# Optimization experiments

Hardware: AMD Instinct MI355X
Metric: run time of the kernel (lower is better)

Reference implementation:

```python
import jax, jax.numpy as jnp
import numpy as np

K = 3
STRIDE = 1
PAD = 1
DIL = 1


def _conv(x, w, b):
    # x: [B,C,H,W], w: [O,C,K,K] (OIHW)
    y = jax.lax.conv_general_dilated(
        x, w, window_strides=(STRIDE, STRIDE),
        padding=[(PAD, PAD), (PAD, PAD)],
        dimension_numbers=("NCHW", "OIHW", "NCHW"))
    return y + b[None, :, None, None]


def _bilinear(img, py, px):
    # img: [B,C,H,W]; py,px: [B,Ho,Wo] float sample coords; zero outside.
    B, C, H, W = img.shape
    y0 = jnp.floor(py)
    x0 = jnp.floor(px)
    wy = py - y0
    wx = px - x0

    def gather(yi, xi):
        valid = (yi >= 0) & (yi < H) & (xi >= 0) & (xi < W)
        yc = jnp.clip(yi, 0, H - 1).astype(jnp.int32)
        xc = jnp.clip(xi, 0, W - 1).astype(jnp.int32)
        v = jax.vmap(lambda im, yy, xx: im[:, yy, xx])(img, yc, xc)  # [B,C,Ho,Wo]
        return v * valid[:, None, :, :].astype(img.dtype)

    v00 = gather(y0, x0)
    v01 = gather(y0, x0 + 1)
    v10 = gather(y0 + 1, x0)
    v11 = gather(y0 + 1, x0 + 1)
    wy_ = wy[:, None]
    wx_ = wx[:, None]
    return ((1 - wy_) * (1 - wx_) * v00 + (1 - wy_) * wx_ * v01
            + wy_ * (1 - wx_) * v10 + wy_ * wx_ * v11)


def setup_inputs() -> dict:
    key = jax.random.key(0)
    ks = jax.random.split(key, 7)
    B, Cin, Cout, H, W = 16, 96, 96, 128, 128
    n = Cin * K * K
    stdv = 1.0 / np.sqrt(n)
    x = jax.random.normal(ks[0], (B, Cin, H, W), jnp.float32)
    weight = jax.random.uniform(ks[1], (Cout, Cin, K, K), jnp.float32, -stdv, stdv)
    bias = jnp.zeros((Cout,), jnp.float32)
    # offset/mask convs: small random weights so sampling offsets are nontrivial
    offset_w = jax.random.normal(ks[2], (2 * K * K, Cin, K, K), jnp.float32) * 0.01
    offset_b = jax.random.normal(ks[3], (2 * K * K,), jnp.float32) * 0.1
    mask_w = jax.random.normal(ks[4], (K * K, Cin, K, K), jnp.float32) * 0.01
    mask_b = jnp.zeros((K * K,), jnp.float32)
    return {"x": x, "weight": weight, "bias": bias,
            "offset_w": offset_w, "offset_b": offset_b,
            "mask_w": mask_w, "mask_b": mask_b}


def reference(x, weight, bias, offset_w, offset_b, mask_w, mask_b):
    offset = _conv(x, offset_w, offset_b)              # [B, 2*K*K, Ho, Wo]
    mask = jax.nn.sigmoid(_conv(x, mask_w, mask_b))    # [B, K*K, Ho, Wo]
    B, C, H, W = x.shape
    Ho, Wo = offset.shape[2], offset.shape[3]
    base_y = (jnp.arange(Ho) * STRIDE - PAD).astype(x.dtype)  # output-row base coord
    base_x = (jnp.arange(Wo) * STRIDE - PAD).astype(x.dtype)
    out = jnp.zeros((B, weight.shape[0], Ho, Wo), x.dtype)
    for k in range(K * K):  # fixed small loop over kernel taps
        i, j = k // K, k % K
        dy = offset[:, 2 * k]      # torchvision ordering: (dy, dx) per tap
        dx = offset[:, 2 * k + 1]
        py = base_y[None, :, None] + i * DIL + dy   # [B,Ho,Wo]
        px = base_x[None, None, :] + j * DIL + dx
        samp = _bilinear(x, py, px) * mask[:, k][:, None]  # [B,C,Ho,Wo]
        out = out + jnp.einsum("bchw,oc->bohw", samp, weight[:, :, i, j])
    return out + bias[None, :, None, None]
```

## Files before the change

### kernel.cpp

```cpp
#include <hip/hip_runtime.h>
#include <math.h>

#define W 128
#define H 128
#define HW 16384
#define CIN 96
#define COUT 96
#define BATCH 16
#define NPIX (BATCH * HW)
#define BPITCH 104
#define BTAP (COUT * BPITCH)
#define BSTG 10240
#define NOT (27 * 32 * 32)

typedef __bf16 bf16x8 __attribute__((ext_vector_type(8)));
typedef float f32x4 __attribute__((ext_vector_type(4)));
typedef unsigned int u32x4 __attribute__((ext_vector_type(4)));

typedef const unsigned int __attribute__((address_space(1))) gu32;
typedef unsigned int __attribute__((address_space(3))) lu32;
#define GLDS16(g, l) __builtin_amdgcn_global_load_lds((gu32*)(g), (lu32*)(l), 16, 0, 0)

__device__ inline float bflo(unsigned d) { union { unsigned u; float f; } t; t.u = d << 16; return t.f; }
__device__ inline float bfhi(unsigned d) { union { unsigned u; float f; } t; t.u = d & 0xffff0000u; return t.f; }

__global__ void prep_weights(const float* __restrict__ weight,
                             const float* __restrict__ offset_w,
                             const float* __restrict__ mask_w,
                             __bf16* __restrict__ wOT,
                             __bf16* __restrict__ wBTp) {
  int idx = blockIdx.x * blockDim.x + threadIdx.x;
  if (idx < NOT) {
    int c = idx & 31;
    int o = (idx >> 5) & 31;
    int ks = idx >> 10;
    int tap = ks / 3;
    int cg = (ks % 3) * 32 + c;
    float v = 0.f;
    if (o < 18)      v = offset_w[(o * CIN + cg) * 9 + tap];
    else if (o < 27) v = mask_w[((o - 18) * CIN + cg) * 9 + tap];
    wOT[idx] = (__bf16)v;
  } else {
    int j = idx - NOT;
    if (j < 9 * BTAP + 256) {
      int c = j % BPITCH;
      int o = (j / BPITCH) % COUT;
      int tap = j / BTAP;
      float v = 0.f;
      if (tap < 9 && c < CIN) v = weight[(o * CIN + c) * 9 + tap];
      wBTp[j] = (__bf16)v;
    }
  }
}

__global__ __launch_bounds__(256) void nhwc_kernel(const float* __restrict__ x,
                                                   __bf16* __restrict__ xT) {
  int tid = blockIdx.x * 256 + threadIdx.x;
  int b = tid >> 14, pix = tid & (HW - 1);
  const float* xp = x + (size_t)b * CIN * HW + pix;
  __bf16* op = xT + (size_t)tid * CIN;
#pragma unroll
  for (int c0 = 0; c0 < CIN; c0 += 8) {
    bf16x8 v;
#pragma unroll
    for (int j = 0; j < 8; ++j) v[j] = (__bf16)xp[(size_t)(c0 + j) * HW];
    *(bf16x8*)(op + c0) = v;
  }
}

#define OISS_TAP(TAP, G) {                                                    \
    int ki = (TAP) / 3, kj = (TAP) % 3;                                       \
    int yy = h + ki - 1, xx = wg + kj - 1;                                    \
    bool ok = ((unsigned)yy < (unsigned)H) && ((unsigned)xx < (unsigned)W);   \
    unsigned vo = ok ? (unsigned)((yy * W + xx) * 192) + choff : 0x7f000000u; \
    asm volatile("buffer_load_dwordx4 %0, %1, %2, %3 offen"                   \
                 : "=v"(G[0]) : "v"(vo), "s"(rsrcX), "s"(0));                 \
    asm volatile("buffer_load_dwordx4 %0, %1, %2, %3 offen"                   \
                 : "=v"(G[1]) : "v"(vo), "s"(rsrcX), "s"(64));                \
    asm volatile("buffer_load_dwordx4 %0, %1, %2, %3 offen"                   \
                 : "=v"(G[2]) : "v"(vo), "s"(rsrcX), "s"(128));               \
  }

#define OISS_B(TAP)                                                           \
  _Pragma("unroll") for (int s = 0; s < 3; ++s)                               \
  _Pragma("unroll") for (int nt = 0; nt < 2; ++nt)                            \
    asm volatile("buffer_load_dwordx4 %0, %1, %2, %3 offen"                   \
                 : "=v"(bb[s * 2 + nt])                                       \
                 : "v"(voffB), "s"(rsrcW),                                    \
                   "s"((TAP) * 6144 + s * 2048 + nt * 1024));

#define OCOMP(GC)                                                             \
  _Pragma("unroll") for (int s = 0; s < 3; ++s) {                             \
    bf16x8 a = __builtin_bit_cast(bf16x8, GC[s]);                             \
    acc[0] = __builtin_amdgcn_mfma_f32_16x16x32_bf16(                         \
        a, __builtin_bit_cast(bf16x8, bb[s * 2 + 0]), acc[0], 0, 0, 0);       \
    acc[1] = __builtin_amdgcn_mfma_f32_16x16x32_bf16(                         \
        a, __builtin_bit_cast(bf16x8, bb[s * 2 + 1]), acc[1], 0, 0, 0);       \
  }

__global__ __launch_bounds__(256) void offmask_mfma(
    const __bf16* __restrict__ xT, const __bf16* __restrict__ wOT,
    const float* __restrict__ offset_b, const float* __restrict__ mask_b,
    float* __restrict__ offm) {
  int t = threadIdx.x;
  int lane = t & 63;
  int wv = __builtin_amdgcn_readfirstlane(t >> 6);
  int ln15 = lane & 15;

  int bid = (int)blockIdx.x;
  int nb = (bid & 7) * 512 + (bid >> 3);
  int b = nb >> 8;
  int rem = nb & 255;
  int h = rem >> 1;
  int w0 = (rem & 1) << 6;

  int pl = (wv << 4) + ln15;
  int wg = w0 + pl;
  unsigned choff = (unsigned)((lane >> 4) << 4);

  const __bf16* xb = xT + (size_t)b * HW * CIN;

  unsigned long long ba = (unsigned long long)(const void*)xb;
  u32x4 rsrcX;
  rsrcX.x = (unsigned)ba; rsrcX.y = (unsigned)(ba >> 32);
  rsrcX.z = (unsigned)(HW * 192);
  rsrcX.w = 0x00020000u;
  unsigned long long bwo = (unsigned long long)(const void*)wOT;
  u32x4 rsrcW;
  rsrcW.x = (unsigned)bwo; rsrcW.y = (unsigned)(bwo >> 32);
  rsrcW.z = (unsigned)(NOT * 2);
  rsrcW.w = 0x00020000u;
  unsigned voffB = (unsigned)(ln15 * 64 + ((lane >> 4) << 4));

  f32x4 acc[2];
  acc[0] = (f32x4){0.f, 0.f, 0.f, 0.f};
  acc[1] = (f32x4){0.f, 0.f, 0.f, 0.f};

  u32x4 gA[3], gB[3], bb[6];

  OISS_TAP(0, gA);
#pragma unroll
  for (int tap = 0; tap < 9; ++tap) {
    OISS_B(tap);
    if (tap < 8) {
      if (tap & 1) { OISS_TAP(tap + 1, gA); } else { OISS_TAP(tap + 1, gB); }
      asm volatile("s_waitcnt vmcnt(3)" ::: "memory");
    } else {
      asm volatile("s_waitcnt vmcnt(0)" ::: "memory");
    }
    __builtin_amdgcn_sched_barrier(0);
    if (tap & 1) { OCOMP(gB); } else { OCOMP(gA); }
  }

  float* ob = offm + (size_t)b * 27 * HW + (size_t)h * W;
  int prow = w0 + (wv << 4) + ((lane >> 4) << 2);
  {
    float bv = offset_b[ln15];
    float4 o4;
    o4.x = acc[0][0] + bv; o4.y = acc[0][1] + bv;
    o4.z = acc[0][2] + bv; o4.w = acc[0][3] + bv;
    *(float4*)(ob + (size_t)ln15 * HW + prow) = o4;
  }
  if (ln15 < 11) {
    int o = 16 + ln15;
    bool sig = (o >= 18);
    float bv = sig ? mask_b[o - 18] : offset_b[o];
    float4 o4;
    float v0 = acc[1][0] + bv, v1 = acc[1][1] + bv;
    float v2 = acc[1][2] + bv, v3 = acc[1][3] + bv;
    if (sig) {
      v0 = 1.f / (1.f + expf(-v0)); v1 = 1.f / (1.f + expf(-v1));
      v2 = 1.f / (1.f + expf(-v2)); v3 = 1.f / (1.f + expf(-v3));
    }
    o4.x = v0; o4.y = v1; o4.z = v2; o4.w = v3;
    *(float4*)(ob + (size_t)o * HW + prow) = o4;
  }
}

#define GISS(K, G, WD) {                                                      \
    float dyv = offt[2 * (K)][pl];                                            \
    float dxv = offt[2 * (K) + 1][pl];                                        \
    float mv  = offt[18 + (K)][pl];                                           \
    int ki = (K) / 3, kj = (K) % 3;                                           \
    float py = (float)(h - 1 + ki) + dyv;                                     \
    float px = (float)(wg - 1 + kj) + dxv;                                    \
    float fy = floorf(py), fx = floorf(px);                                   \
    float wyf = py - fy, wxf = px - fx;                                       \
    int iy0 = (int)fy, ix0 = (int)fx;                                         \
    int iy1 = iy0 + 1, ix1 = ix0 + 1;                                         \
    bool y0ok = (unsigned)iy0 < (unsigned)H;                                  \
    bool y1ok = (unsigned)iy1 < (unsigned)H;                                  \
    bool x0ok = (unsigned)ix0 < (unsigned)W;                                  \
    bool x1ok = (unsigned)ix1 < (unsigned)W;                                  \
    WD[0] = (y0ok && x0ok) ? (1.f - wyf) * (1.f - wxf) * mv : 0.f;            \
    WD[1] = (y0ok && x1ok) ? (1.f - wyf) * wxf * mv : 0.f;                    \
    WD[2] = (y1ok && x0ok) ? wyf * (1.f - wxf) * mv : 0.f;                    \
    WD[3] = (y1ok && x1ok) ? wyf * wxf * mv : 0.f;                            \
    int cy0 = min(max(iy0, 0), H - 1), cy1 = min(max(iy1, 0), H - 1);         \
    int cx0 = min(max(ix0, 0), W - 1), cx1 = min(max(ix1, 0), W - 1);         \
    unsigned v00 = (unsigned)((cy0 * W + cx0) * 192) + choff;                 \
    unsigned v01 = (unsigned)((cy0 * W + cx1) * 192) + choff;                 \
    unsigned v10 = (unsigned)((cy1 * W + cx0) * 192) + choff;                 \
    unsigned v11 = (unsigned)((cy1 * W + cx1) * 192) + choff;                 \
    _Pragma("unroll") for (int ks = 0; ks < 3; ++ks) {                        \
      asm volatile("buffer_load_dwordx4 %0, %1, %2, %3 offen"                 \
                   : "=v"(G[ks * 4 + 0]) : "v"(v00), "s"(rsrcX), "s"(ks * 64)); \
      asm volatile("buffer_load_dwordx4 %0, %1, %2, %3 offen"                 \
                   : "=v"(G[ks * 4 + 1]) : "v"(v01), "s"(rsrcX), "s"(ks * 64)); \
      asm volatile("buffer_load_dwordx4 %0, %1, %2, %3 offen"                 \
                   : "=v"(G[ks * 4 + 2]) : "v"(v10), "s"(rsrcX), "s"(ks * 64)); \
      asm volatile("buffer_load_dwordx4 %0, %1, %2, %3 offen"                 \
                   : "=v"(G[ks * 4 + 3]) : "v"(v11), "s"(rsrcX), "s"(ks * 64)); \
    } }

#define COMBINE_KS(G, KS, WV, AF)                                             \
  _Pragma("unroll") for (int j = 0; j < 8; ++j) {                             \
    unsigned d00 = G[(KS) * 4 + 0][j >> 1], d01 = G[(KS) * 4 + 1][j >> 1];    \
    unsigned d10 = G[(KS) * 4 + 2][j >> 1], d11 = G[(KS) * 4 + 3][j >> 1];    \
    float v00 = (j & 1) ? bfhi(d00) : bflo(d00);                              \
    float v01 = (j & 1) ? bfhi(d01) : bflo(d01);                              \
    float v10 = (j & 1) ? bfhi(d10) : bflo(d10);                              \
    float v11 = (j & 1) ? bfhi(d11) : bflo(d11);                              \
    AF[j] = (__bf16)(WV[0] * v00 + WV[1] * v01 + WV[2] * v10 + WV[3] * v11);  \
  }

#define STAGE_B(K, BUF) {                                                     \
    const __bf16* src = wBTp + (size_t)(K) * BTAP + (size_t)wv * 2560 +       \
                        (size_t)lane * 8;                                     \
    __bf16* dst = (BUF) + wv * 2560;                                          \
    _Pragma("unroll") for (int q = 0; q < 5; ++q)                             \
      GLDS16(src + q * 512, dst + q * 512);                                   \
  }

__global__ __launch_bounds__(256, 3) void deform_kernel(
    const __bf16* __restrict__ xT, const float* __restrict__ offm,
    const __bf16* __restrict__ wBTp, const float* __restrict__ bias,
    float* __restrict__ out) {
  __shared__ alignas(16) __bf16 Blds[2][BSTG];
  __shared__ float offt[27][64];

  int t = threadIdx.x;
  int lane = t & 63;
  int wv = __builtin_amdgcn_readfirstlane(t >> 6);
  int ln15 = lane & 15;

  int bid = (int)blockIdx.x;
  int nb = (bid & 7) * 512 + (bid >> 3);
  int b = nb >> 8;
  int rem = nb & 255;
  int h = rem >> 1;
  int w0 = (rem & 1) << 6;

  int pl = (wv << 4) + ln15;
  int wg = w0 + pl;
  unsigned choff = (unsigned)((lane >> 4) << 4);

  const __bf16* xb = xT + (size_t)b * HW * CIN;
  const float* ob = offm + (size_t)b * 27 * HW;

  unsigned long long ba = (unsigned long long)(const void*)xb;
  u32x4 rsrcX;
  rsrcX.x = (unsigned)ba; rsrcX.y = (unsigned)(ba >> 32);
  rsrcX.z = 0xffffffffu;  rsrcX.w = 0x00020000u;

  for (int e = t; e < 27 * 64; e += 256) {
    int o = e >> 6, p = e & 63;
    offt[o][p] = ob[(size_t)o * HW + (size_t)h * W + w0 + p];
  }
  STAGE_B(0, &Blds[0][0]);
  __syncthreads();

  f32x4 acc[6];
#pragma unroll
  for (int nt = 0; nt < 6; ++nt) acc[nt] = (f32x4){0.f, 0.f, 0.f, 0.f};

  u32x4 g[12];
  f32x4 wd;

  GISS(0, g, wd);
  STAGE_B(1, &Blds[1][0]);

  for (int k = 0; k < 9; ++k) {
    const __bf16* bfrag = &Blds[k & 1][0] + (size_t)ln15 * BPITCH + ((lane >> 4) << 3);

    if (k < 8) { asm volatile("s_waitcnt vmcnt(5)" ::: "memory"); }
    else       { asm volatile("s_waitcnt vmcnt(0)" ::: "memory"); }
    __builtin_amdgcn_sched_barrier(0);

    bf16x8 af0, af1, af2;
    COMBINE_KS(g, 0, wd, af0);
    COMBINE_KS(g, 1, wd, af1);
    COMBINE_KS(g, 2, wd, af2);

    if (k < 8) { GISS(k + 1, g, wd); }

#pragma unroll
    for (int nt = 0; nt < 6; ++nt) {
      const __bf16* bp = bfrag + nt * 16 * BPITCH;
      bf16x8 b0 = *(const bf16x8*)(bp);
      bf16x8 b1 = *(const bf16x8*)(bp + 32);
      bf16x8 b2 = *(const bf16x8*)(bp + 64);
      acc[nt] = __builtin_amdgcn_mfma_f32_16x16x32_bf16(af0, b0, acc[nt], 0, 0, 0);
      acc[nt] = __builtin_amdgcn_mfma_f32_16x16x32_bf16(af1, b1, acc[nt], 0, 0, 0);
      acc[nt] = __builtin_amdgcn_mfma_f32_16x16x32_bf16(af2, b2, acc[nt], 0, 0, 0);
    }

    if (k < 8) {
      __syncthreads();
      if (k < 7) STAGE_B(k + 2, &Blds[k & 1][0]);
    }
  }

  float* outb = out + (size_t)b * COUT * HW + (size_t)h * W;
  int prow = w0 + (wv << 4) + ((lane >> 4) << 2);
#pragma unroll
  for (int nt = 0; nt < 6; ++nt) {
    int ch = nt * 16 + ln15;
    float bv = bias[ch];
    float4 o4;
    o4.x = acc[nt][0] + bv;
    o4.y = acc[nt][1] + bv;
    o4.z = acc[nt][2] + bv;
    o4.w = acc[nt][3] + bv;
    *(float4*)(outb + (size_t)ch * HW + prow) = o4;
  }
}

extern "C" void kernel_launch(void* const* d_in, const int* in_sizes, int n_in,
                              void* d_out, int out_size, void* d_ws, size_t ws_size,
                              hipStream_t stream) {
  const float* x        = (const float*)d_in[0];
  const float* weight   = (const float*)d_in[1];
  const float* bias     = (const float*)d_in[2];
  const float* offset_w = (const float*)d_in[3];
  const float* offset_b = (const float*)d_in[4];
  const float* mask_w   = (const float*)d_in[5];
  const float* mask_b   = (const float*)d_in[6];
  float* out = (float*)d_out;

  __bf16* xT   = (__bf16*)d_ws;
  float*  offm = (float*)(xT + (size_t)NPIX * CIN);
  __bf16* wOT  = (__bf16*)(offm + (size_t)BATCH * 27 * HW);
  __bf16* wBTp = wOT + NOT;

  const int nPrep = NOT + 9 * BTAP + 256;
  prep_weights<<<(nPrep + 255) / 256, 256, 0, stream>>>(weight, offset_w, mask_w, wOT, wBTp);
  nhwc_kernel<<<NPIX / 256, 256, 0, stream>>>(x, xT);
  offmask_mfma<<<BATCH * H * (W / 64), 256, 0, stream>>>(xT, wOT, offset_b, mask_b, offm);
  deform_kernel<<<BATCH * H * (W / 64), 256, 0, stream>>>(xT, offm, wBTp, bias, out);
}
```

Before: 294.2 us.

## Prefetch offsets per-thread via buffer loads and restructure tap pipeline

Drops the shared-memory staging of the offset/mask tile. Each thread now loads its own dy, dx and mask values with buffer loads issued two taps ahead. The 9-tap loop is fully unrolled, and the weight tile for the next tap is staged into double-buffered LDS each iteration instead of two taps ahead. The goal is to remove the upfront offset copy and barrier and to overlap more global traffic with MFMA work. In exchange, the explicit vmcnt waits inside the loop are gone, so correctness and overlap now depend on how the barriers drain outstanding loads.

```diff
diff --git a/kernel.cpp b/kernel.cpp
--- a/kernel.cpp
+++ b/kernel.cpp
@@ -177,13 +177,19 @@
   }
 }
 
-#define GISS(K, G, WD) {                                                      \
-    float dyv = offt[2 * (K)][pl];                                            \
-    float dxv = offt[2 * (K) + 1][pl];                                        \
-    float mv  = offt[18 + (K)][pl];                                           \
+#define OFFL(K, DY, DX, MM) {                                                 \
+    asm volatile("buffer_load_dword %0, %1, %2, %3 offen"                     \
+                 : "=v"(DY) : "v"(voffP), "s"(rsrcO), "s"((2 * (K)) * (HW * 4))); \
+    asm volatile("buffer_load_dword %0, %1, %2, %3 offen"                     \
+                 : "=v"(DX) : "v"(voffP), "s"(rsrcO), "s"((2 * (K) + 1) * (HW * 4))); \
+    asm volatile("buffer_load_dword %0, %1, %2, %3 offen"                     \
+                 : "=v"(MM) : "v"(voffP), "s"(rsrcO), "s"((18 + (K)) * (HW * 4))); \
+  }
+
+#define GISS(K, G, WD, DYV, DXV, MV) {                                        \
     int ki = (K) / 3, kj = (K) % 3;                                           \
-    float py = (float)(h - 1 + ki) + dyv;                                     \
-    float px = (float)(wg - 1 + kj) + dxv;                                    \
+    float py = (float)(h - 1 + ki) + (DYV);                                   \
+    float px = (float)(wg - 1 + kj) + (DXV);                                  \
     float fy = floorf(py), fx = floorf(px);                                   \
     float wyf = py - fy, wxf = px - fx;                                       \
     int iy0 = (int)fy, ix0 = (int)fx;                                         \
@@ -192,10 +198,10 @@
     bool y1ok = (unsigned)iy1 < (unsigned)H;                                  \
     bool x0ok = (unsigned)ix0 < (unsigned)W;                                  \
     bool x1ok = (unsigned)ix1 < (unsigned)W;                                  \
-    WD[0] = (y0ok && x0ok) ? (1.f - wyf) * (1.f - wxf) * mv : 0.f;            \
-    WD[1] = (y0ok && x1ok) ? (1.f - wyf) * wxf * mv : 0.f;                    \
-    WD[2] = (y1ok && x0ok) ? wyf * (1.f - wxf) * mv : 0.f;                    \
-    WD[3] = (y1ok && x1ok) ? wyf * wxf * mv : 0.f;                            \
+    WD[0] = (y0ok && x0ok) ? (1.f - wyf) * (1.f - wxf) * (MV) : 0.f;          \
+    WD[1] = (y0ok && x1ok) ? (1.f - wyf) * wxf * (MV) : 0.f;                  \
+    WD[2] = (y1ok && x0ok) ? wyf * (1.f - wxf) * (MV) : 0.f;                  \
+    WD[3] = (y1ok && x1ok) ? wyf * wxf * (MV) : 0.f;                          \
     int cy0 = min(max(iy0, 0), H - 1), cy1 = min(max(iy1, 0), H - 1);         \
     int cx0 = min(max(ix0, 0), W - 1), cx1 = min(max(ix1, 0), W - 1);         \
     unsigned v00 = (unsigned)((cy0 * W + cx0) * 192) + choff;                 \
@@ -227,9 +233,35 @@
 #define STAGE_B(K, BUF) {                                                     \
     const __bf16* src = wBTp + (size_t)(K) * BTAP + (size_t)wv * 2560 +       \
                         (size_t)lane * 8;                                     \
-    __bf16* dst = (BUF) + wv * 2560;                                          \
+    __bf16* dst = (BUF) + wv * 2560;                                         \
     _Pragma("unroll") for (int q = 0; q < 5; ++q)                             \
       GLDS16(src + q * 512, dst + q * 512);                                   \
+  }
+
+#define MFMA_TAP(BUFIDX) {                                                    \
+    const __bf16* bfrag = &Blds[BUFIDX][0] + (size_t)ln15 * BPITCH +          \
+                          ((lane >> 4) << 3);                                 \
+    _Pragma("unroll") for (int nt = 0; nt < 6; ++nt) {                        \
+      const __bf16* bp = bfrag + nt * 16 * BPITCH;                            \
+      bf16x8 b0 = *(const bf16x8*)(bp);                                       \
+      bf16x8 b1 = *(const bf16x8*)(bp + 32);                                  \
+      bf16x8 b2 = *(const bf16x8*)(bp + 64);                                  \
+      acc[nt] = __builtin_amdgcn_mfma_f32_16x16x32_bf16(af0, b0, acc[nt], 0, 0, 0); \
+      acc[nt] = __builtin_amdgcn_mfma_f32_16x16x32_bf16(af1, b1, acc[nt], 0, 0, 0); \
+      acc[nt] = __builtin_amdgcn_mfma_f32_16x16x32_bf16(af2, b2, acc[nt], 0, 0, 0); \
+    } }
+
+#define ITER(K, DYN, DXN, MN, DYF, DXF, MF) {                                 \
+    bf16x8 af0, af1, af2;                                                     \
+    COMBINE_KS(g, 0, wd, af0);                                                \
+    COMBINE_KS(g, 1, wd, af1);                                                \
+    COMBINE_KS(g, 2, wd, af2);                                                \
+    GISS((K) + 1, g, wd, DYN, DXN, MN);                                       \
+    if ((K) <= 6) { OFFL((K) + 2, DYF, DXF, MF); }                            \
+    STAGE_B((K) + 1, &Blds[((K) + 1) & 1][0]);                                \
+    MFMA_TAP((K) & 1);                                                        \
+    __syncthreads();                                                          \
+    __builtin_amdgcn_sched_barrier(0);                                        \
   }
 
 __global__ __launch_bounds__(256, 3) void deform_kernel(
@@ -237,7 +269,6 @@
     const __bf16* __restrict__ wBTp, const float* __restrict__ bias,
     float* __restrict__ out) {
   __shared__ alignas(16) __bf16 Blds[2][BSTG];
-  __shared__ float offt[27][64];
 
   int t = threadIdx.x;
   int lane = t & 63;
@@ -262,13 +293,11 @@
   u32x4 rsrcX;
   rsrcX.x = (unsigned)ba; rsrcX.y = (unsigned)(ba >> 32);
   rsrcX.z = 0xffffffffu;  rsrcX.w = 0x00020000u;
-
-  for (int e = t; e < 27 * 64; e += 256) {
-    int o = e >> 6, p = e & 63;
-    offt[o][p] = ob[(size_t)o * HW + (size_t)h * W + w0 + p];
-  }
-  STAGE_B(0, &Blds[0][0]);
-  __syncthreads();
+  unsigned long long bo = (unsigned long long)(const void*)ob;
+  u32x4 rsrcO;
+  rsrcO.x = (unsigned)bo; rsrcO.y = (unsigned)(bo >> 32);
+  rsrcO.z = 0xffffffffu;  rsrcO.w = 0x00020000u;
+  unsigned voffP = (unsigned)((h * W + wg) * 4);
 
   f32x4 acc[6];
 #pragma unroll
@@ -276,39 +305,32 @@
 
   u32x4 g[12];
   f32x4 wd;
-
-  GISS(0, g, wd);
-  STAGE_B(1, &Blds[1][0]);
-
-  for (int k = 0; k < 9; ++k) {
-    const __bf16* bfrag = &Blds[k & 1][0] + (size_t)ln15 * BPITCH + ((lane >> 4) << 3);
-
-    if (k < 8) { asm volatile("s_waitcnt vmcnt(5)" ::: "memory"); }
-    else       { asm volatile("s_waitcnt vmcnt(0)" ::: "memory"); }
-    __builtin_amdgcn_sched_barrier(0);
-
+  float dy0, dx0, m0, dy1, dx1, m1;
+
+  OFFL(0, dy0, dx0, m0);
+  OFFL(1, dy1, dx1, m1);
+  STAGE_B(0, &Blds[0][0]);
+  asm volatile("s_waitcnt vmcnt(8)" ::: "memory");
+  __builtin_amdgcn_sched_barrier(0);
+  GISS(0, g, wd, dy0, dx0, m0);
+  __syncthreads();
+  __builtin_amdgcn_sched_barrier(0);
+
+  ITER(0, dy1, dx1, m1, dy0, dx0, m0);
+  ITER(1, dy0, dx0, m0, dy1, dx1, m1);
+  ITER(2, dy1, dx1, m1, dy0, dx0, m0);
+  ITER(3, dy0, dx0, m0, dy1, dx1, m1);
+  ITER(4, dy1, dx1, m1, dy0, dx0, m0);
+  ITER(5, dy0, dx0, m0, dy1, dx1, m1);
+  ITER(6, dy1, dx1, m1, dy0, dx0, m0);
+  ITER(7, dy0, dx0, m0, dy1, dx1, m1);
+
+  {
     bf16x8 af0, af1, af2;
     COMBINE_KS(g, 0, wd, af0);
     COMBINE_KS(g, 1, wd, af1);
     COMBINE_KS(g, 2, wd, af2);
-
-    if (k < 8) { GISS(k + 1, g, wd); }
-
-#pragma unroll
-    for (int nt = 0; nt < 6; ++nt) {
-      const __bf16* bp = bfrag + nt * 16 * BPITCH;
-      bf16x8 b0 = *(const bf16x8*)(bp);
-      bf16x8 b1 = *(const bf16x8*)(bp + 32);
-      bf16x8 b2 = *(const bf16x8*)(bp + 64);
-      acc[nt] = __builtin_amdgcn_mfma_f32_16x16x32_bf16(af0, b0, acc[nt], 0, 0, 0);
-      acc[nt] = __builtin_amdgcn_mfma_f32_16x16x32_bf16(af1, b1, acc[nt], 0, 0, 0);
-      acc[nt] = __builtin_amdgcn_mfma_f32_16x16x32_bf16(af2, b2, acc[nt], 0, 0, 0);
-    }
-
-    if (k < 8) {
-      __syncthreads();
-      if (k < 7) STAGE_B(k + 2, &Blds[k & 1][0]);
-    }
+    MFMA_TAP(0);
   }
 
   float* outb = out + (size_t)b * COUT * HW + (size_t)h * W;
```

New measurement: 285.9 us. -2.8%, faster.
